# Kernel tuning notes

Hardware: AMD Instinct MI355X
Metric: run time of the kernel (lower is better)

The kernel has to match this reference:

```python
import jax, jax.numpy as jnp
import numpy as np

B, N, E, S, A, P, T = 512, 65536, 131072, 256, 512, 2, 64


def setup_inputs() -> dict:
    key = jax.random.key(0)
    ks = jax.random.split(key, 40)
    f32 = jnp.float32

    def g(i, shape, s=0.05):
        return jax.random.normal(ks[i], shape, f32) * s

    inp = {
        'nodes': jax.random.normal(ks[0], (N, S), f32),
        'edge_features': jax.random.normal(ks[1], (E, S), f32),
        'edge_source': jax.random.randint(ks[2], (E,), 0, N),
        'edge_dest': jax.random.randint(ks[3], (E,), 0, N),
        'node_owner': jax.random.randint(ks[4], (N,), 0, B),
        'running': jnp.ones((B,), bool),
        'ref_types': jax.random.randint(ks[5], (B,), 0, T),
        # decision aggregator (transform + sigmoid gate)
        'dec_t_W': g(6, (A, S)), 'dec_t_b': g(7, (A,)),
        'dec_g_W': g(8, (A, S)), 'dec_g_b': jnp.ones((A,), f32),
        # init aggregator
        'init_t_W': g(9, (A, S)), 'init_t_b': g(10, (A,)),
        'init_g_W': g(11, (A, S)), 'init_g_b': jnp.ones((A,), f32),
        # node type decision head + embedding
        'ntd_W': g(12, (T + 1, A)), 'ntd_b': g(13, (T + 1,)),
        'nte': g(14, (T, S), 1.0),
        # f_init
        'f1_W': g(15, (S, S)), 'f1_b': g(16, (S,)),
        'f2_W': g(17, (S, A)),
        # propagator params, stacked over P steps (message_size = 2S)
        'mn_W': g(18, (P, 2 * S, S)),
        'mf_W': g(19, (P, 2 * S, S)),
        'ml2_W': g(20, (P, 2 * S, 2 * S)), 'ml2_b': g(21, (P, 2 * S)),
        'gru_Wih': g(22, (P, 3 * S, 2 * S)), 'gru_Whh': g(23, (P, 3 * S, S)),
        'gru_bih': jnp.zeros((P, 3 * S), f32),
        'gru_bhh': jnp.concatenate(
            [jnp.ones((P, S), f32), jnp.zeros((P, 2 * S), f32)], axis=-1),
    }
    return inp


def _aggregate(nodes, fmask, tW, tb, gW, gb):
    # Aggregator.forward: sigmoid gate * linear transform, pooled per graph
    # via dense 0/1 owner-mask matmul (dropout=0 -> identity).
    gates = jax.nn.sigmoid(nodes @ gW.T + gb)
    data = nodes @ tW.T + tb
    return fmask @ (data * gates)  # [B, A]


def reference(nodes, edge_features, edge_source, edge_dest, node_owner,
              running, ref_types,
              dec_t_W, dec_t_b, dec_g_W, dec_g_b,
              init_t_W, init_t_b, init_g_W, init_g_b,
              ntd_W, ntd_b, nte, f1_W, f1_b, f2_W,
              mn_W, mf_W, ml2_W, ml2_b, gru_Wih, gru_Whh, gru_bih, gru_bhh):
    f32 = nodes.dtype
    fmask = (node_owner[None, :] == jnp.arange(B)[:, None]).astype(f32)  # [B,N]
    # Propagator._node_update_mask: owner_masks[running].sum(0) > 0
    upd = (fmask * running[:, None].astype(f32)).sum(0) > 0  # [N]

    for p in range(P):
        ef = edge_features @ mf_W[p].T                 # [E, 2S]
        nf = nodes @ mn_W[p].T                         # [N, 2S]
        msgs = nf[edge_source] + nf[edge_dest] + ef
        msgs = jnp.tanh(msgs) @ ml2_W[p].T + ml2_b[p]  # message_layer_2
        inputs = jnp.zeros((N, 2 * S), f32)
        inputs = inputs.at[edge_dest].add(msgs).at[edge_source].add(msgs)
        # torch GRUCell (gate order r, z, n)
        gi = inputs @ gru_Wih[p].T + gru_bih[p]
        gh = nodes @ gru_Whh[p].T + gru_bhh[p]
        ir, iz, inn = jnp.split(gi, 3, axis=-1)
        hr, hz, hn = jnp.split(gh, 3, axis=-1)
        r = jax.nn.sigmoid(ir + hr)
        z = jax.nn.sigmoid(iz + hz)
        n = jnp.tanh(inn + r * hn)
        new_nodes = (1.0 - z) * n + z * nodes
        nodes = jnp.where(upd[:, None], new_nodes, nodes)

    # node-type decision
    agg = _aggregate(nodes, fmask, dec_t_W, dec_t_b, dec_g_W, dec_g_b)
    logits = agg @ ntd_W.T + ntd_b                      # [B, T+1]

    # training path: remap_pad (no pad chars present) -> ref + 1
    sel = ref_types + 1                                  # in [1, T]
    logp = jax.nn.log_softmax(logits, axis=-1)
    per_ex = -logp[jnp.arange(B), sel]
    loss = jnp.where(running, per_ex, 0.0).mean()

    # new node features for running graphs
    emb = nte[sel - 1]                                   # [B, S]
    init_feats = _aggregate(nodes, fmask, init_t_W, init_t_b,
                            init_g_W, init_g_b)
    new_features = emb @ f1_W.T + f1_b + init_feats @ f2_W.T  # [B, S]
    return logits, new_features, loss
```

## Files before the change

### kernel.cpp

```cpp
#include <hip/hip_runtime.h>
#include <hip/hip_bf16.h>
#include <math.h>

#define BG 512
#define NN 65536
#define EE 131072
#define SD 256
#define AD 512
#define PP 2
#define TD 64

typedef __attribute__((ext_vector_type(8))) short sx8;
typedef __attribute__((ext_vector_type(4))) short sx4;
typedef __attribute__((ext_vector_type(4))) float fx4;

__device__ __forceinline__ float bs2f(short s) {
    union { unsigned u; float f; } x; x.u = ((unsigned)(unsigned short)s) << 16; return x.f;
}
__device__ __forceinline__ short f2bs(float f) {
    union { float f; unsigned u; } x; x.f = f;
    unsigned r = x.u + 0x7fffu + ((x.u >> 16) & 1u);
    return (short)(r >> 16);
}
__device__ __forceinline__ float fast_tanh(float x) {
    float xc = fminf(fmaxf(x, -15.f), 15.f);
    float e = __expf(2.f * xc);
    return __fdividef(e - 1.f, e + 1.f);
}
__device__ __forceinline__ float fast_sigm(float x) {
    float xc = fminf(fmaxf(x, -30.f), 30.f);
    float e = __expf(-xc);
    return __fdividef(1.f, 1.f + e);
}
__device__ __forceinline__ bool run_flag(const void* runv, int idx) {
    const unsigned char* r8 = (const unsigned char*)runv;
    const int* r32 = (const int*)runv;
    return (r8[idx] != 0) || (r32[idx] != 0);
}

__device__ __forceinline__ void gload16(const short* g, short* l) {
    __builtin_amdgcn_global_load_lds(
        (const __attribute__((address_space(1))) void*)g,
        (__attribute__((address_space(3))) void*)l, 16, 0, 0);
}

template<int EPI>
__launch_bounds__(256, 4)
__global__ void gemm_bt(const short* __restrict__ Abp, const short* __restrict__ Abp2,
                        const short* __restrict__ Wp,
                        const float* __restrict__ bias, const float* __restrict__ bias2,
                        short* __restrict__ Cout, short* __restrict__ Fout,
                        short* __restrict__ FoutB,
                        const float* __restrict__ biasB, const float* __restrict__ biasB2,
                        int K, int Ksp, int NC, int NT, int nsplit)
{
    __shared__ __align__(16) short sA[2 * 4096];
    __shared__ __align__(16) short sB[2 * 4096];
    const int t = threadIdx.x;
    const int lane = t & 63;
    const int w = t >> 6;

    const int nwg = gridDim.x;
    const int q = nwg >> 3;
    const int wg = (blockIdx.x & 7) * q + (blockIdx.x >> 3);
    const int mt = wg / NT;
    const int nt = wg - mt * NT;
    const int m0 = mt * 128;
    const int n0 = nt * 128;

    const int wm = (w >> 1) * 64;
    const int wn = (w & 1) * 64;
    const int lr = lane & 15;
    const int lg = lane >> 4;

    fx4 acc[4][4];
#pragma unroll
    for (int i = 0; i < 4; i++)
#pragma unroll
        for (int j = 0; j < 4; j++) { fx4 z = {0.f, 0.f, 0.f, 0.f}; acc[i][j] = z; }

    const int r = t >> 2;
    const int cblk = (t & 3) ^ ((r >> 1) & 3);
    const short* gA  = Abp  + (size_t)(m0 + r) * Ksp + cblk * 8;
    const short* gA2 = Abp2 + (size_t)(m0 + r) * (K - Ksp) + cblk * 8;
    const short* gB  = Wp + (size_t)(n0 + r) * K + cblk * 8;
    const size_t rsA  = (size_t)64 * Ksp;
    const size_t rsA2 = (size_t)64 * (K - Ksp);
    const size_t rsB  = (size_t)64 * K;

    auto STAGE = [&](int b, int kk) {
        const short* a0 = (kk < Ksp) ? (gA + kk) : (gA2 + (kk - Ksp));
        const size_t rs = (kk < Ksp) ? rsA : rsA2;
        gload16(a0,            sA + b * 4096 + w * 512);
        gload16(a0 + rs,       sA + b * 4096 + 2048 + w * 512);
        gload16(gB + kk,       sB + b * 4096 + w * 512);
        gload16(gB + kk + rsB, sB + b * 4096 + 2048 + w * 512);
    };

    STAGE(0, 0);
    __syncthreads();
    int buf = 0;
    const int xa = (lr >> 1) & 3;
    for (int kk = 0; kk < K; kk += 32) {
        if (kk + 32 < K) STAGE(buf ^ 1, kk + 32);
        const short* cA = sA + buf * 4096;
        const short* cB = sB + buf * 4096;
        sx8 af[4], bfr[4];
#pragma unroll
        for (int mi = 0; mi < 4; mi++)
            af[mi] = *(const sx8*)(cA + (wm + mi * 16 + lr) * 32 + (lg ^ xa) * 8);
#pragma unroll
        for (int ni = 0; ni < 4; ni++)
            bfr[ni] = *(const sx8*)(cB + (wn + ni * 16 + lr) * 32 + (lg ^ xa) * 8);
#pragma unroll
        for (int mi = 0; mi < 4; mi++)
#pragma unroll
            for (int ni = 0; ni < 4; ni++) {
                if (EPI == 4)
                    acc[mi][ni] = __builtin_amdgcn_mfma_f32_16x16x32_bf16(
                        af[mi], bfr[ni], acc[mi][ni], 0, 0, 0);
                else
                    acc[mi][ni] = __builtin_amdgcn_mfma_f32_16x16x32_bf16(
                        bfr[ni], af[mi], acc[mi][ni], 0, 0, 0);
            }
        __syncthreads();
        buf ^= 1;
    }

    if (EPI == 4) {
        const bool useB = (n0 >= nsplit);
        short* fo = useB ? FoutB : Fout;
        const float* tb = useB ? biasB : bias;
        const float* gb = useB ? biasB2 : bias2;
        const int ln0 = useB ? (n0 - nsplit) : n0;
#pragma unroll
        for (int mi = 0; mi < 4; mi++) {
#pragma unroll
            for (int rg = 0; rg < 4; rg++) {
                const int m = m0 + wm + mi * 16 + lg * 4 + rg;
#pragma unroll
                for (int ni = 0; ni < 4; ni += 2) {
                    const int rc = (((ln0 + wn + ni * 16) >> 5) << 4) + lr;
                    float dv = acc[mi][ni][rg] + tb[rc];
                    float gv = fast_sigm(acc[mi][ni + 1][rg] + gb[rc]);
                    fo[(size_t)m * 512 + rc] = f2bs(dv * gv);
                }
            }
        }
    } else {
#pragma unroll
        for (int mi = 0; mi < 4; mi++) {
            const int m = m0 + wm + mi * 16 + lr;
            short* co = Cout + (size_t)m * NC + n0;
#pragma unroll
            for (int ni = 0; ni < 4; ni++) {
                const int nc = wn + ni * 16 + lg * 4;
                sx4 o;
                if (EPI == 1) {
#pragma unroll
                    for (int rg = 0; rg < 4; rg++)
                        o[rg] = f2bs(fast_tanh(acc[mi][ni][rg]));
                } else {
                    fx4 vb = {0.f, 0.f, 0.f, 0.f};
                    if (bias) vb = *(const fx4*)(bias + n0 + nc);
#pragma unroll
                    for (int rg = 0; rg < 4; rg++)
                        o[rg] = f2bs(acc[mi][ni][rg] + vb[rg]);
                }
                *(sx4*)(co + nc) = o;
            }
        }
    }
}

__global__ void k_xadd(const short* __restrict__ nodes, const int* __restrict__ esrc,
                       const int* __restrict__ edst, short* __restrict__ X)
{
    size_t idx = ((size_t)blockIdx.x * 256 + threadIdx.x) * 8;
    const int e = (int)(idx >> 8);
    const int j = (int)(idx & 255);
    const int s = esrc[e], d = edst[e];
    sx8 a = *(const sx8*)(nodes + (size_t)s * 256 + j);
    sx8 b = *(const sx8*)(nodes + (size_t)d * 256 + j);
    sx8 o;
#pragma unroll
    for (int u = 0; u < 8; u++) o[u] = f2bs(bs2f(a[u]) + bs2f(b[u]));
    *(sx8*)(X + idx) = o;
}

__global__ void k_castw(const float* __restrict__ in, short* __restrict__ out)
{
    size_t i = ((size_t)blockIdx.x * 256 + threadIdx.x) * 4;
    fx4 v = *(const fx4*)(in + i);
    sx4 o;
#pragma unroll
    for (int u = 0; u < 4; u++) o[u] = f2bs(v[u]);
    *(sx4*)(out + i) = o;
}

__global__ void k_cast_comb(const float* __restrict__ mn, const float* __restrict__ mf,
                            short* __restrict__ out)
{
    size_t i = ((size_t)blockIdx.x * 256 + threadIdx.x) * 4;
    const int n = (int)(i >> 9);
    const int k = (int)(i & 511);
    const float* W = (k < 256) ? (mn + (size_t)n * 256 + k)
                               : (mf + (size_t)n * 256 + (k - 256));
    fx4 v = *(const fx4*)W;
    sx4 o;
#pragma unroll
    for (int u = 0; u < 4; u++) o[u] = f2bs(v[u]);
    *(sx4*)(out + i) = o;
}

__global__ void k_cast_pair(const float* __restrict__ tW, const float* __restrict__ gW,
                            short* __restrict__ out)
{
    size_t i = ((size_t)blockIdx.x * 256 + threadIdx.x) * 4;
    const int r2 = (int)(i >> 8);
    const int c = (int)(i & 255);
    const int src = ((r2 >> 5) << 4) | (r2 & 15);
    const float* W = ((r2 >> 4) & 1) ? gW : tW;
    fx4 v = *(const fx4*)(W + (size_t)src * 256 + c);
    sx4 o;
#pragma unroll
    for (int u = 0; u < 4; u++) o[u] = f2bs(v[u]);
    *(sx4*)(out + i) = o;
}

__global__ void k_count2(const int* __restrict__ a, const int* __restrict__ b,
                         int* __restrict__ deg, int n)
{
    int i = blockIdx.x * 256 + threadIdx.x;
    if (i < n) { atomicAdd(&deg[a[i]], 1); atomicAdd(&deg[b[i]], 1); }
}
__global__ void k_count1(const int* __restrict__ a, int* __restrict__ deg, int n)
{
    int i = blockIdx.x * 256 + threadIdx.x;
    if (i < n) atomicAdd(&deg[a[i]], 1);
}
__global__ void k_scan(const int* __restrict__ deg, int* __restrict__ offs, int n)
{
    __shared__ int part[256];
    const int t = threadIdx.x;
    const int chunk = n >> 8;
    const int base = t * chunk;
    int s = 0;
    for (int i = 0; i < chunk; i++) s += deg[base + i];
    part[t] = s;
    __syncthreads();
    for (int off = 1; off < 256; off <<= 1) {
        int v = (t >= off) ? part[t - off] : 0;
        __syncthreads();
        part[t] += v;
        __syncthreads();
    }
    int run = (t > 0) ? part[t - 1] : 0;
    for (int i = 0; i < chunk; i++) {
        offs[base + i] = run;
        run += deg[base + i];
    }
    if (t == 255) offs[n] = part[255];
}
__global__ void k_fill2(const int* __restrict__ a, const int* __restrict__ b,
                        const int* __restrict__ offs, int* __restrict__ cur,
                        int* __restrict__ elist, int n)
{
    int i = blockIdx.x * 256 + threadIdx.x;
    if (i < n) {
        int p = atomicAdd(&cur[a[i]], 1); elist[offs[a[i]] + p] = i;
        int q = atomicAdd(&cur[b[i]], 1); elist[offs[b[i]] + q] = i;
    }
}
__global__ void k_fill1(const int* __restrict__ own, const int* __restrict__ offs,
                        int* __restrict__ cur, int* __restrict__ nlist, int n)
{
    int i = blockIdx.x * 256 + threadIdx.x;
    if (i < n) {
        int p = atomicAdd(&cur[own[i]], 1); nlist[offs[own[i]] + p] = i;
    }
}

__global__ void k_edge_gather(const short* __restrict__ msgs, const int* __restrict__ offs,
                              const int* __restrict__ elist, short* __restrict__ inp)
{
    const int node = blockIdx.x * 4 + (threadIdx.x >> 6);
    const int c = (threadIdx.x & 63) * 8;
    const int s0 = offs[node], s1 = offs[node + 1];
    float acc[8] = {0.f, 0.f, 0.f, 0.f, 0.f, 0.f, 0.f, 0.f};
    for (int s = s0; s < s1; s++) {
        const int e = elist[s];
        sx8 v = *(const sx8*)(msgs + (size_t)e * 512 + c);
#pragma unroll
        for (int u = 0; u < 8; u++) acc[u] += bs2f(v[u]);
    }
    sx8 o;
#pragma unroll
    for (int u = 0; u < 8; u++) o[u] = f2bs(acc[u]);
    *(sx8*)(inp + (size_t)node * 512 + c) = o;
}

__global__ void k_owner_reduce(const short* __restrict__ gp, const int* __restrict__ offsB,
                               const int* __restrict__ nlist, float* __restrict__ agg)
{
    const int b = blockIdx.x, t = threadIdx.x;
    const int s0 = offsB[b], s1 = offsB[b + 1];
    float a0 = 0.f, a1 = 0.f;
    for (int s = s0; s < s1; s++) {
        const int n = nlist[s];
        const short* pp = gp + (size_t)n * 512 + t * 2;
        a0 += bs2f(pp[0]); a1 += bs2f(pp[1]);
    }
    agg[(size_t)b * 512 + t * 2] = a0;
    agg[(size_t)b * 512 + t * 2 + 1] = a1;
}

__global__ void k_gru(const short* __restrict__ gi, const short* __restrict__ gh,
                      short* __restrict__ nodes,
                      const int* __restrict__ owner, const void* __restrict__ runv)
{
    const int n = blockIdx.x * 4 + (threadIdx.x >> 6);
    const int t = threadIdx.x & 63;
    const bool run = run_flag(runv, owner[n]);
    const size_t gb = (size_t)n * 768 + t * 4;
    sx4 vir = *(const sx4*)(gi + gb);
    sx4 viz = *(const sx4*)(gi + gb + 256);
    sx4 vin = *(const sx4*)(gi + gb + 512);
    sx4 whr = *(const sx4*)(gh + gb);
    sx4 whz = *(const sx4*)(gh + gb + 256);
    sx4 whn = *(const sx4*)(gh + gb + 512);
    const size_t nbase = (size_t)n * 256 + t * 4;
    sx4 old4 = *(const sx4*)(nodes + nbase);
    sx4 outb;
#pragma unroll
    for (int u = 0; u < 4; u++) {
        float old = bs2f(old4[u]);
        float rr = fast_sigm(bs2f(vir[u]) + bs2f(whr[u]));
        float zz = fast_sigm(bs2f(viz[u]) + bs2f(whz[u]));
        float nn = fast_tanh(bs2f(vin[u]) + rr * bs2f(whn[u]));
        float nv = (1.f - zz) * nn + zz * old;
        outb[u] = run ? f2bs(nv) : old4[u];
    }
    *(sx4*)(nodes + nbase) = outb;
}

__global__ void k_logits(const float* __restrict__ agg, const float* __restrict__ Wt,
                         const float* __restrict__ bt, float* __restrict__ logitsF,
                         float* __restrict__ outL)
{
    __shared__ float row[512];
    const int b = blockIdx.x, t = threadIdx.x;
    for (int k = t; k < 512; k += 128) row[k] = agg[(size_t)b * 512 + k];
    __syncthreads();
    if (t < TD + 1) {
        float acc = bt[t];
        const float* wr = Wt + (size_t)t * 512;
        for (int k = 0; k < 512; k++) acc += row[k] * wr[k];
        logitsF[b * (TD + 1) + t] = acc;
        outL[b * (TD + 1) + t] = acc;
    }
}

__global__ void k_loss(const float* __restrict__ logitsF, const int* __restrict__ reft,
                       const void* __restrict__ runv, float* __restrict__ outLoss)
{
    __shared__ float red[512];
    const int b = threadIdx.x;
    const float* lr = logitsF + b * (TD + 1);
    float mx = lr[0];
    for (int k = 1; k < TD + 1; k++) mx = fmaxf(mx, lr[k]);
    float se = 0.f;
    for (int k = 0; k < TD + 1; k++) se += expf(lr[k] - mx);
    const int sel = reft[b] + 1;
    float pe = logf(se) + mx - lr[sel];
    red[b] = run_flag(runv, b) ? pe : 0.f;
    __syncthreads();
    for (int s = 256; s > 0; s >>= 1) {
        if (b < s) red[b] += red[b + s];
        __syncthreads();
    }
    if (b == 0) outLoss[0] = red[0] / (float)BG;
}

__global__ void k_newfeat(const float* __restrict__ aggi, const float* __restrict__ nte,
                          const int* __restrict__ reft, const float* __restrict__ f1W,
                          const float* __restrict__ f1b, const float* __restrict__ f2W,
                          float* __restrict__ outNF)
{
    __shared__ float emb[256];
    __shared__ float ag[512];
    const int b = blockIdx.x, t = threadIdx.x;
    const int rt = reft[b];
    emb[t] = nte[(size_t)rt * 256 + t];
    ag[t] = aggi[(size_t)b * 512 + t];
    ag[t + 256] = aggi[(size_t)b * 512 + 256 + t];
    __syncthreads();
    float acc = f1b[t];
    const float* w1 = f1W + (size_t)t * 256;
    for (int k = 0; k < 256; k++) acc += emb[k] * w1[k];
    const float* w2 = f2W + (size_t)t * 512;
    for (int a = 0; a < 512; a++) acc += ag[a] * w2[a];
    outNF[(size_t)b * 256 + t] = acc;
}

extern "C" void kernel_launch(void* const* d_in, const int* in_sizes, int n_in,
                              void* d_out, int out_size, void* d_ws, size_t ws_size,
                              hipStream_t stream)
{
    (void)in_sizes; (void)n_in; (void)out_size;
    const float* in_nodes = (const float*)d_in[0];
    const float* in_ef    = (const float*)d_in[1];
    const int*   e_src    = (const int*)d_in[2];
    const int*   e_dst    = (const int*)d_in[3];
    const int*   owner    = (const int*)d_in[4];
    const void*  running  = d_in[5];
    const int*   reft     = (const int*)d_in[6];
    const float* dec_tW = (const float*)d_in[7];
    const float* dec_tb = (const float*)d_in[8];
    const float* dec_gW = (const float*)d_in[9];
    const float* dec_gb = (const float*)d_in[10];
    const float* init_tW = (const float*)d_in[11];
    const float* init_tb = (const float*)d_in[12];
    const float* init_gW = (const float*)d_in[13];
    const float* init_gb = (const float*)d_in[14];
    const float* ntdW = (const float*)d_in[15];
    const float* ntdb = (const float*)d_in[16];
    const float* nte  = (const float*)d_in[17];
    const float* f1W  = (const float*)d_in[18];
    const float* f1b  = (const float*)d_in[19];
    const float* f2W  = (const float*)d_in[20];
    const float* mnW  = (const float*)d_in[21];
    const float* mfW  = (const float*)d_in[22];
    const float* ml2W = (const float*)d_in[23];
    const float* ml2b = (const float*)d_in[24];
    const float* Wih  = (const float*)d_in[25];
    const float* Whh  = (const float*)d_in[26];
    const float* bih  = (const float*)d_in[27];
    const float* bhh  = (const float*)d_in[28];

    float* outL    = (float*)d_out;
    float* outNF   = outL + BG * (TD + 1);
    float* outLoss = outNF + BG * SD;

    size_t off = 0;
    auto take = [&](size_t bytes) -> void* {
        void* p = (char*)d_ws + off;
        off += (bytes + 255) & ~(size_t)255;
        return p;
    };
    short* nodes_bf  = (short*)take((size_t)NN * SD * 2);
    short* ef_bf     = (short*)take((size_t)EE * SD * 2);
    short* bufC      = (short*)take((size_t)EE * SD * 2);
    short* bufD      = (short*)take((size_t)EE * 512 * 2);
    short* bufM      = (short*)take((size_t)EE * 512 * 2);
    short* bufI      = (short*)take((size_t)NN * 512 * 2);
    float* aggD      = (float*)take((size_t)BG * AD * 4);
    float* aggI      = (float*)take((size_t)BG * AD * 4);
    float* logitsF   = (float*)take((size_t)BG * (TD + 1) * 4);
    short* WcombB = (short*)take((size_t)PP * 512 * 512 * 2);
    short* ml2Wb = (short*)take((size_t)PP * 512 * 512 * 2);
    short* WihB  = (short*)take((size_t)PP * 768 * 512 * 2);
    short* WhhB  = (short*)take((size_t)PP * 768 * 256 * 2);
    short* W4agg = (short*)take((size_t)2048 * 256 * 2);
    int* deg_e = (int*)take((size_t)NN * 4);
    int* offs_e = (int*)take((size_t)(NN + 1) * 4);
    int* cur_e = (int*)take((size_t)NN * 4);
    int* elist = (int*)take((size_t)2 * EE * 4);
    int* degB = (int*)take((size_t)BG * 4);
    int* offsB = (int*)take((size_t)(BG + 1) * 4);
    int* curB = (int*)take((size_t)BG * 4);
    int* nlist = (int*)take((size_t)NN * 4);
    if (off > ws_size) return;

    short* gi = bufD;
    short* gh = bufM;
    short* gpD = bufM;
    short* gpI = bufD;

    k_castw<<<NN * SD / 1024, 256, 0, stream>>>(in_nodes, nodes_bf);
    k_castw<<<EE * SD / 1024, 256, 0, stream>>>(in_ef, ef_bf);
    for (int p = 0; p < PP; p++)
        k_cast_comb<<<512 * 512 / 1024, 256, 0, stream>>>(
            mnW + (size_t)p * 512 * 256, mfW + (size_t)p * 512 * 256,
            WcombB + (size_t)p * 512 * 512);
    k_castw<<<PP * 512 * 512 / 1024, 256, 0, stream>>>(ml2W, ml2Wb);
    k_castw<<<PP * 768 * 512 / 1024, 256, 0, stream>>>(Wih, WihB);
    k_castw<<<PP * 768 * 256 / 1024, 256, 0, stream>>>(Whh, WhhB);
    k_cast_pair<<<1024 * 256 / 1024, 256, 0, stream>>>(dec_tW, dec_gW, W4agg);
    k_cast_pair<<<1024 * 256 / 1024, 256, 0, stream>>>(init_tW, init_gW,
                                                       W4agg + 1024 * 256);

    hipMemsetAsync(deg_e, 0, (size_t)NN * 4, stream);
    hipMemsetAsync(cur_e, 0, (size_t)NN * 4, stream);
    hipMemsetAsync(degB, 0, (size_t)BG * 4, stream);
    hipMemsetAsync(curB, 0, (size_t)BG * 4, stream);
    k_count2<<<(EE + 255) / 256, 256, 0, stream>>>(e_src, e_dst, deg_e, EE);
    k_scan<<<1, 256, 0, stream>>>(deg_e, offs_e, NN);
    k_fill2<<<(EE + 255) / 256, 256, 0, stream>>>(e_src, e_dst, offs_e, cur_e, elist, EE);
    k_count1<<<(NN + 255) / 256, 256, 0, stream>>>(owner, degB, NN);
    k_scan<<<1, 256, 0, stream>>>(degB, offsB, BG);
    k_fill1<<<(NN + 255) / 256, 256, 0, stream>>>(owner, offsB, curB, nlist, NN);

    for (int p = 0; p < PP; p++) {
        k_xadd<<<EE / 8, 256, 0, stream>>>(nodes_bf, e_src, e_dst, bufC);
        gemm_bt<1><<<EE / 128 * 4, 256, 0, stream>>>(
            bufC, ef_bf, WcombB + (size_t)p * 512 * 512, nullptr, nullptr,
            bufD, nullptr, nullptr, nullptr, nullptr,
            512, 256, 512, 4, 0);
        gemm_bt<0><<<EE / 128 * 4, 256, 0, stream>>>(
            bufD, bufD, ml2Wb + (size_t)p * 512 * 512, ml2b + (size_t)p * 512,
            nullptr, bufM, nullptr, nullptr, nullptr, nullptr,
            512, 512, 512, 4, 0);
        k_edge_gather<<<NN / 4, 256, 0, stream>>>(bufM, offs_e, elist, bufI);
        gemm_bt<0><<<NN / 128 * 6, 256, 0, stream>>>(
            bufI, bufI, WihB + (size_t)p * 768 * 512, bih + (size_t)p * 768,
            nullptr, gi, nullptr, nullptr, nullptr, nullptr,
            512, 512, 768, 6, 0);
        gemm_bt<0><<<NN / 128 * 6, 256, 0, stream>>>(
            nodes_bf, nodes_bf, WhhB + (size_t)p * 768 * 256, bhh + (size_t)p * 768,
            nullptr, gh, nullptr, nullptr, nullptr, nullptr,
            256, 256, 768, 6, 0);
        k_gru<<<NN / 4, 256, 0, stream>>>(gi, gh, nodes_bf, owner, running);
    }

    gemm_bt<4><<<NN / 128 * 16, 256, 0, stream>>>(
        nodes_bf, nodes_bf, W4agg, dec_tb, dec_gb,
        nullptr, gpD, gpI, init_tb, init_gb,
        256, 256, 2048, 16, 1024);
    k_owner_reduce<<<BG, 256, 0, stream>>>(gpD, offsB, nlist, aggD);
    k_owner_reduce<<<BG, 256, 0, stream>>>(gpI, offsB, nlist, aggI);

    k_logits<<<BG, 128, 0, stream>>>(aggD, ntdW, ntdb, logitsF, outL);
    k_loss<<<1, 512, 0, stream>>>(logitsF, reft, running, outLoss);
    k_newfeat<<<BG, 256, 0, stream>>>(aggI, nte, reft, f1W, f1b, f2W, outNF);
}
```

Before: 1.821 ms.

## Fold ml2 linear layer into GRU input weights via linearity of edge aggregation

The per-edge ml2 linear layer (E x 512 x 512 GEMM) is removed by precomputing Wih·ml2W as a fused weight and Wih·ml2b as a vector scaled by node degree. This works because the scatter-sum over edges is linear and sits between the two layers. The node-level GEMM then uses the fused weight, with an epilogue that adds degree times the fused bias. This drops one large edge GEMM per step in exchange for small setup GEMMs and an extra bf16 rounding of the fused weights, which may change numerics.

```diff
diff --git a/kernel.cpp b/kernel.cpp
--- a/kernel.cpp
+++ b/kernel.cpp
@@ -52,6 +52,7 @@
                         short* __restrict__ Cout, short* __restrict__ Fout,
                         short* __restrict__ FoutB,
                         const float* __restrict__ biasB, const float* __restrict__ biasB2,
+                        const int* __restrict__ degp,
                         int K, int Ksp, int NC, int NT, int nsplit)
 {
     __shared__ __align__(16) short sA[2 * 4096];
@@ -98,6 +99,14 @@
     };
 
     STAGE(0, 0);
+
+    float dgv[4];
+    if (EPI == 3) {
+#pragma unroll
+        for (int mi = 0; mi < 4; mi++)
+            dgv[mi] = (float)degp[m0 + wm + mi * 16 + lr];
+    }
+
     __syncthreads();
     int buf = 0;
     const int xa = (lr >> 1) & 3;
@@ -160,6 +169,12 @@
 #pragma unroll
                     for (int rg = 0; rg < 4; rg++)
                         o[rg] = f2bs(fast_tanh(acc[mi][ni][rg]));
+                } else if (EPI == 3) {
+                    fx4 bv = *(const fx4*)(bias + n0 + nc);
+                    fx4 cv = *(const fx4*)(bias2 + n0 + nc);
+#pragma unroll
+                    for (int rg = 0; rg < 4; rg++)
+                        o[rg] = f2bs(acc[mi][ni][rg] + dgv[mi] * cv[rg] + bv[rg]);
                 } else {
                     fx4 vb = {0.f, 0.f, 0.f, 0.f};
                     if (bias) vb = *(const fx4*)(bias + n0 + nc);
@@ -196,6 +211,28 @@
 #pragma unroll
     for (int u = 0; u < 4; u++) o[u] = f2bs(v[u]);
     *(sx4*)(out + i) = o;
+}
+
+__global__ void k_cast_T(const float* __restrict__ in, short* __restrict__ out)
+{
+    size_t i = ((size_t)blockIdx.x * 256 + threadIdx.x) * 4;
+    const int k = (int)(i >> 9);
+    const int k2 = (int)(i & 511);
+    sx4 o;
+#pragma unroll
+    for (int u = 0; u < 4; u++) o[u] = f2bs(in[(size_t)(k2 + u) * 512 + k]);
+    *(sx4*)(out + i) = o;
+}
+
+__global__ void k_vecfuse(const float* __restrict__ Wih, const float* __restrict__ ml2b,
+                          float* __restrict__ c1)
+{
+    const int i = blockIdx.x * 256 + threadIdx.x;
+    if (i >= 768) return;
+    const float* wr = Wih + (size_t)i * 512;
+    float acc = 0.f;
+    for (int k = 0; k < 512; k++) acc += wr[k] * ml2b[k];
+    c1[i] = acc;
 }
 
 __global__ void k_cast_comb(const float* __restrict__ mn, const float* __restrict__ mf,
@@ -458,7 +495,9 @@
     float* aggI      = (float*)take((size_t)BG * AD * 4);
     float* logitsF   = (float*)take((size_t)BG * (TD + 1) * 4);
     short* WcombB = (short*)take((size_t)PP * 512 * 512 * 2);
-    short* ml2Wb = (short*)take((size_t)PP * 512 * 512 * 2);
+    short* ml2Tb  = (short*)take((size_t)512 * 512 * 2);
+    short* WfB    = (short*)take((size_t)PP * 768 * 512 * 2);
+    float* c1f    = (float*)take((size_t)PP * 768 * 4);
     short* WihB  = (short*)take((size_t)PP * 768 * 512 * 2);
     short* WhhB  = (short*)take((size_t)PP * 768 * 256 * 2);
     short* W4agg = (short*)take((size_t)2048 * 256 * 2);
@@ -483,12 +522,22 @@
         k_cast_comb<<<512 * 512 / 1024, 256, 0, stream>>>(
             mnW + (size_t)p * 512 * 256, mfW + (size_t)p * 512 * 256,
             WcombB + (size_t)p * 512 * 512);
-    k_castw<<<PP * 512 * 512 / 1024, 256, 0, stream>>>(ml2W, ml2Wb);
     k_castw<<<PP * 768 * 512 / 1024, 256, 0, stream>>>(Wih, WihB);
     k_castw<<<PP * 768 * 256 / 1024, 256, 0, stream>>>(Whh, WhhB);
     k_cast_pair<<<1024 * 256 / 1024, 256, 0, stream>>>(dec_tW, dec_gW, W4agg);
     k_cast_pair<<<1024 * 256 / 1024, 256, 0, stream>>>(init_tW, init_gW,
                                                        W4agg + 1024 * 256);
+    for (int p = 0; p < PP; p++) {
+        k_cast_T<<<512 * 512 / 1024, 256, 0, stream>>>(
+            ml2W + (size_t)p * 512 * 512, ml2Tb);
+        gemm_bt<0><<<768 / 128 * 4, 256, 0, stream>>>(
+            WihB + (size_t)p * 768 * 512, WihB + (size_t)p * 768 * 512, ml2Tb,
+            nullptr, nullptr, WfB + (size_t)p * 768 * 512,
+            nullptr, nullptr, nullptr, nullptr, nullptr,
+            512, 512, 512, 4, 0);
+        k_vecfuse<<<3, 256, 0, stream>>>(Wih + (size_t)p * 768 * 512,
+                                         ml2b + (size_t)p * 512, c1f + p * 768);
+    }
 
     hipMemsetAsync(deg_e, 0, (size_t)NN * 4, stream);
     hipMemsetAsync(cur_e, 0, (size_t)NN * 4, stream);
@@ -505,27 +554,24 @@
         k_xadd<<<EE / 8, 256, 0, stream>>>(nodes_bf, e_src, e_dst, bufC);
         gemm_bt<1><<<EE / 128 * 4, 256, 0, stream>>>(
             bufC, ef_bf, WcombB + (size_t)p * 512 * 512, nullptr, nullptr,
-            bufD, nullptr, nullptr, nullptr, nullptr,
+            bufD, nullptr, nullptr, nullptr, nullptr, nullptr,
             512, 256, 512, 4, 0);
-        gemm_bt<0><<<EE / 128 * 4, 256, 0, stream>>>(
-            bufD, bufD, ml2Wb + (size_t)p * 512 * 512, ml2b + (size_t)p * 512,
-            nullptr, bufM, nullptr, nullptr, nullptr, nullptr,
-            512, 512, 512, 4, 0);
-        k_edge_gather<<<NN / 4, 256, 0, stream>>>(bufM, offs_e, elist, bufI);
-        gemm_bt<0><<<NN / 128 * 6, 256, 0, stream>>>(
-            bufI, bufI, WihB + (size_t)p * 768 * 512, bih + (size_t)p * 768,
-            nullptr, gi, nullptr, nullptr, nullptr, nullptr,
+        k_edge_gather<<<NN / 4, 256, 0, stream>>>(bufD, offs_e, elist, bufI);
+        gemm_bt<3><<<NN / 128 * 6, 256, 0, stream>>>(
+            bufI, bufI, WfB + (size_t)p * 768 * 512,
+            bih + (size_t)p * 768, c1f + p * 768,
+            gi, nullptr, nullptr, nullptr, nullptr, deg_e,
             512, 512, 768, 6, 0);
         gemm_bt<0><<<NN / 128 * 6, 256, 0, stream>>>(
             nodes_bf, nodes_bf, WhhB + (size_t)p * 768 * 256, bhh + (size_t)p * 768,
-            nullptr, gh, nullptr, nullptr, nullptr, nullptr,
+            nullptr, gh, nullptr, nullptr, nullptr, nullptr, nullptr,
             256, 256, 768, 6, 0);
         k_gru<<<NN / 4, 256, 0, stream>>>(gi, gh, nodes_bf, owner, running);
     }
 
     gemm_bt<4><<<NN / 128 * 16, 256, 0, stream>>>(
         nodes_bf, nodes_bf, W4agg, dec_tb, dec_gb,
-        nullptr, gpD, gpI, init_tb, init_gb,
+        nullptr, gpD, gpI, init_tb, init_gb, nullptr,
         256, 256, 2048, 16, 1024);
     k_owner_reduce<<<BG, 256, 0, stream>>>(gpD, offsB, nlist, aggD);
     k_owner_reduce<<<BG, 256, 0, stream>>>(gpI, offsB, nlist, aggI);
```

Measured after the change: 1.659 ms. -8.9%, faster.
